# Kernel tuning notes

Hardware: AMD Instinct MI355X
Metric: run time of the kernel (lower is better)

## Reference

```python
import jax, jax.numpy as jnp
import numpy as np


def trilinear_sample(x, pts):
    """F.grid_sample 3D, mode='bilinear' (trilinear), padding_mode='border', align_corners=True.
    x: [B,C,D,H,W]; pts: [B,P,3] normalized coords in (x,y,z)=(W,H,D) order. Returns [B,C,P]."""
    B, C, D, H, W = x.shape

    def unnorm(g, size):
        # align_corners=True mapping, border padding = clamp coordinate
        return jnp.clip((g + 1.0) * 0.5 * (size - 1), 0.0, size - 1.0)

    ix = unnorm(pts[..., 0], W)
    iy = unnorm(pts[..., 1], H)
    iz = unnorm(pts[..., 2], D)
    x0 = jnp.floor(ix); y0 = jnp.floor(iy); z0 = jnp.floor(iz)
    fx = (ix - x0)[:, None, :]; fy = (iy - y0)[:, None, :]; fz = (iz - z0)[:, None, :]
    x0i = x0.astype(jnp.int32); y0i = y0.astype(jnp.int32); z0i = z0.astype(jnp.int32)
    x1i = jnp.minimum(x0i + 1, W - 1)
    y1i = jnp.minimum(y0i + 1, H - 1)
    z1i = jnp.minimum(z0i + 1, D - 1)

    xf = x.reshape(B, C, D * H * W)

    def gather(zi, yi, xi):
        idx = (zi * H + yi) * W + xi  # [B,P]
        return jnp.take_along_axis(xf, idx[:, None, :], axis=2)  # [B,C,P]

    wx0 = 1.0 - fx; wx1 = fx
    wy0 = 1.0 - fy; wy1 = fy
    wz0 = 1.0 - fz; wz1 = fz
    out = (gather(z0i, y0i, x0i) * wz0 * wy0 * wx0
           + gather(z0i, y0i, x1i) * wz0 * wy0 * wx1
           + gather(z0i, y1i, x0i) * wz0 * wy1 * wx0
           + gather(z0i, y1i, x1i) * wz0 * wy1 * wx1
           + gather(z1i, y0i, x0i) * wz1 * wy0 * wx0
           + gather(z1i, y0i, x1i) * wz1 * wy0 * wx1
           + gather(z1i, y1i, x0i) * wz1 * wy1 * wx0
           + gather(z1i, y1i, x1i) * wz1 * wy1 * wx1)
    return out


def setup_inputs() -> dict:
    key = jax.random.key(0)
    ks = jax.random.split(key, 12)
    B, C, G, N, K = 2, 64, 64, 50000, 8
    Cin = C + 3          # point_head / neighbour_head input channels
    Cd = C + 3 + 4       # delta conv input channels (features + coords + shape)
    s = 0.05
    x = jax.random.normal(ks[0], (B, C, G, G, G), jnp.float32)
    vertices = jax.random.uniform(ks[1], (B, N, 3), jnp.float32, -1.0, 1.0)
    shape_w = jax.random.normal(ks[2], (4, 4), jnp.float32) * s
    shape_b = jax.random.normal(ks[3], (4,), jnp.float32) * s
    # original init fills delta weights with 0; use small random values for a non-degenerate test
    delta_w = jax.random.normal(ks[4], (K * 3, Cd), jnp.float32) * 0.01
    delta_b = jax.random.normal(ks[5], (K * 3,), jnp.float32) * 0.01
    ph_w = jax.random.normal(ks[6], (C, Cin), jnp.float32) * s
    ph_b = jax.random.normal(ks[7], (C,), jnp.float32) * s
    nh1_w = jax.random.normal(ks[8], (C, Cin), jnp.float32) * s
    nh1_b = jax.random.normal(ks[9], (C,), jnp.float32) * s
    nh2_w = jax.random.normal(ks[10], (C, C, K + 1), jnp.float32) * s  # Conv2d kernel (1, K+1), no bias
    return {"x": x, "vertices": vertices, "shape_w": shape_w, "shape_b": shape_b,
            "delta_w": delta_w, "delta_b": delta_b, "ph_w": ph_w, "ph_b": ph_b,
            "nh1_w": nh1_w, "nh1_b": nh1_b, "nh2_w": nh2_w}


def reference(x, vertices, shape_w, shape_b, delta_w, delta_b, ph_w, ph_b, nh1_w, nh1_b, nh2_w):
    B, C, D, H, W = x.shape
    N = vertices.shape[1]
    K = delta_w.shape[0] // 3

    # sample point features
    xp = trilinear_sample(x, vertices)                                   # [B,C,N]
    cpoints = jnp.concatenate([xp, vertices.transpose(0, 2, 1)], axis=1)  # [B,C+3,N]

    # point head: 1x1 conv == per-point linear
    pfeat = jnp.einsum('oc,bcn->bno', ph_w, cpoints) + ph_b               # [B,N,C]

    # shape conditioning
    shape_vec = jnp.array([C, D, H, W], jnp.float32) @ shape_w.T + shape_b  # [4]
    sfeat = jnp.broadcast_to(shape_vec[None, :, None], (B, 4, N))
    feats = jnp.concatenate([cpoints, sfeat], axis=1)                     # [B,C+7,N]

    # learned neighbour offsets
    delta = (jnp.einsum('oc,bcn->bno', delta_w, feats) + delta_b).reshape(B, N, K, 3)
    nbrs = vertices[:, :, None, :] + delta                                # [B,N,K,3]

    # sample neighbour features
    xn = trilinear_sample(x, nbrs.reshape(B, N * K, 3)).reshape(B, C, N, K)
    cnb = jnp.concatenate([xn, nbrs.transpose(0, 3, 1, 2)], axis=1)       # [B,C+3,N,K]
    nin = jnp.concatenate([cpoints[..., None], cnb], axis=-1)             # [B,C+3,N,K+1]

    # neighbour head: 1x1 conv -> GELU -> (1,K+1) conv (reduces the K+1 axis)
    h = jax.nn.gelu(jnp.einsum('oc,bcnk->bonk', nh1_w, nin)
                    + nh1_b[None, :, None, None], approximate=False)
    nfeat = jnp.einsum('ock,bcnk->bno', nh2_w, h)                         # [B,N,C]

    return pfeat + nfeat
```

## Files before the change

### kernel.cpp

```cpp
#include <hip/hip_runtime.h>
#include <math.h>

constexpr int Bc = 2, Cc = 64, Nc = 50000, Kc = 8;
constexpr int PT = 16;
constexpr int NBLK = (Bc * Nc) / PT;

constexpr int BIAS_PH = 16;
constexpr int BIAS_N1 = 272;
constexpr int BIAS_DL = 528;
constexpr int B_PH  = 1024;
constexpr int B_N1  = 13312;
constexpr int B_DH  = 25600;
constexpr int B_DLO = 31744;
constexpr int B_N2  = 37888;
constexpr size_t XT_BYTE = 262144;
constexpr size_t XT_USHORTS = (size_t)Bc * 64 * 64 * 64 * 64;

using bf16x8 = __attribute__((ext_vector_type(8))) short;
using f32x4  = __attribute__((ext_vector_type(4))) float;

__device__ __forceinline__ float gelu_exact(float v) {
    return 0.5f * v * (1.0f + erff(v * 0.70710678118654752f));
}
__device__ __forceinline__ ushort f2bf(float f) {
    unsigned u = __float_as_uint(f);
    unsigned r = (u + 0x7FFFu + ((u >> 16) & 1u)) >> 16;
    return (ushort)r;
}
__device__ __forceinline__ float bf2f(ushort u) {
    return __uint_as_float(((unsigned)u) << 16);
}
__device__ __forceinline__ float tri8(float v000, float v001, float v010, float v011,
                                      float v100, float v101, float v110, float v111,
                                      float fx, float fy, float fz) {
    float c00 = fmaf(fx, v001 - v000, v000);
    float c01 = fmaf(fx, v011 - v010, v010);
    float c10 = fmaf(fx, v101 - v100, v100);
    float c11 = fmaf(fx, v111 - v110, v110);
    float c0  = fmaf(fy, c01 - c00, c00);
    float c1  = fmaf(fy, c11 - c10, c10);
    return fmaf(fz, c1 - c0, c0);
}

__device__ __forceinline__ void sample_pair(const unsigned* __restrict__ xtb32,
                                            ushort* __restrict__ stage,
                                            int cp, int p,
                                            float nx, float ny, float nz) {
    float ix = fminf(fmaxf((nx + 1.0f) * 31.5f, 0.0f), 63.0f);
    float iy = fminf(fmaxf((ny + 1.0f) * 31.5f, 0.0f), 63.0f);
    float iz = fminf(fmaxf((nz + 1.0f) * 31.5f, 0.0f), 63.0f);
    float fx0 = floorf(ix), fy0 = floorf(iy), fz0 = floorf(iz);
    int x0 = (int)fx0, y0 = (int)fy0, z0 = (int)fz0;
    float fx = ix - fx0, fy = iy - fy0, fz = iz - fz0;
    int dx = (x0 < 63) ? 32 : 0;
    int dy = (y0 < 63) ? 2048 : 0;
    int dz = (z0 < 63) ? 131072 : 0;
    const unsigned* r = xtb32 + ((((z0 << 12) + (y0 << 6) + x0) << 5) + cp);
    unsigned u000 = r[0],       u001 = r[dx];
    unsigned u010 = r[dy],      u011 = r[dy + dx];
    unsigned u100 = r[dz],      u101 = r[dz + dx];
    unsigned u110 = r[dz + dy], u111 = r[dz + dy + dx];
    float sa = tri8(bf2f((ushort)u000), bf2f((ushort)u001),
                    bf2f((ushort)u010), bf2f((ushort)u011),
                    bf2f((ushort)u100), bf2f((ushort)u101),
                    bf2f((ushort)u110), bf2f((ushort)u111), fx, fy, fz);
    float sb = tri8(bf2f((ushort)(u000 >> 16)), bf2f((ushort)(u001 >> 16)),
                    bf2f((ushort)(u010 >> 16)), bf2f((ushort)(u011 >> 16)),
                    bf2f((ushort)(u100 >> 16)), bf2f((ushort)(u101 >> 16)),
                    bf2f((ushort)(u110 >> 16)), bf2f((ushort)(u111 >> 16)), fx, fy, fz);
    *(unsigned*)(stage + p * 104 + 2 * cp) =
        (unsigned)f2bf(sa) | ((unsigned)f2bf(sb) << 16);
}

__device__ __forceinline__ float sample_cm(const float* __restrict__ xb,
                                           float gx, float gy, float gz) {
    float ix = fminf(fmaxf((gx + 1.0f) * 31.5f, 0.0f), 63.0f);
    float iy = fminf(fmaxf((gy + 1.0f) * 31.5f, 0.0f), 63.0f);
    float iz = fminf(fmaxf((gz + 1.0f) * 31.5f, 0.0f), 63.0f);
    float fx0 = floorf(ix), fy0 = floorf(iy), fz0 = floorf(iz);
    int x0 = (int)fx0, y0 = (int)fy0, z0 = (int)fz0;
    float fx = ix - fx0, fy = iy - fy0, fz = iz - fz0;
    int x1 = (x0 < 63) ? x0 + 1 : 63;
    int dy = (y0 < 63) ? 64 : 0;
    int dz = (z0 < 63) ? 4096 : 0;
    const float* r = xb + ((z0 << 12) + (y0 << 6));
    float v000 = r[x0],           v001 = r[x1];
    float v010 = r[x0 + dy],      v011 = r[x1 + dy];
    float v100 = r[x0 + dz],      v101 = r[x1 + dz];
    float v110 = r[x0 + dy + dz], v111 = r[x1 + dy + dz];
    return tri8(v000, v001, v010, v011, v100, v101, v110, v111, fx, fy, fz);
}

__global__ void sb_pack(const float* __restrict__ shape_w, const float* __restrict__ shape_b,
                        const float* __restrict__ delta_w, const float* __restrict__ delta_b,
                        const float* __restrict__ ph_w, const float* __restrict__ ph_b,
                        const float* __restrict__ nh1_w, const float* __restrict__ nh1_b,
                        const float* __restrict__ nh2_w, char* __restrict__ wsb) {
    int tid = blockIdx.x * blockDim.x + threadIdx.x;
    int nt  = gridDim.x * blockDim.x;
    float*  bph = (float*)(wsb + BIAS_PH);
    float*  bn1 = (float*)(wsb + BIAS_N1);
    float*  bdl = (float*)(wsb + BIAS_DL);
    ushort* wph = (ushort*)(wsb + B_PH);
    ushort* wn1 = (ushort*)(wsb + B_N1);
    ushort* wdh = (ushort*)(wsb + B_DH);
    ushort* wdl = (ushort*)(wsb + B_DLO);
    ushort* wn2 = (ushort*)(wsb + B_N2);

    for (int e = tid; e < 64; e += nt) { bph[e] = ph_b[e]; bn1[e] = nh1_b[e]; }
    for (int e = tid; e < 32; e += nt) {
        float v = 0.0f;
        if (e < 24) {
            v = delta_b[e];
#pragma unroll
            for (int i = 0; i < 4; ++i) {
                float sv = 64.0f * (shape_w[i*4] + shape_w[i*4+1] + shape_w[i*4+2] + shape_w[i*4+3])
                         + shape_b[i];
                v += sv * delta_w[e * 71 + 67 + i];
            }
        }
        bdl[e] = v;
    }
    for (int e = tid; e < 6144; e += nt) {
        int frag = e >> 9, lane = (e >> 3) & 63, j = e & 7;
        int kt = frag >> 2, n = frag & 3;
        int k = kt * 32 + ((lane >> 4) << 3) + j;
        int col = n * 16 + (lane & 15);
        wph[e] = (k < 67) ? f2bf(ph_w[col * 67 + k])  : (ushort)0;
        wn1[e] = (k < 67) ? f2bf(nh1_w[col * 67 + k]) : (ushort)0;
    }
    for (int e = tid; e < 3072; e += nt) {
        int frag = e >> 9, lane = (e >> 3) & 63, j = e & 7;
        int kt = frag >> 1, n = frag & 1;
        int k = kt * 32 + ((lane >> 4) << 3) + j;
        int col = n * 16 + (lane & 15);
        float w = (col < 24 && k < 67) ? delta_w[col * 71 + k] : 0.0f;
        ushort hi = f2bf(w);
        wdh[e] = hi;
        wdl[e] = f2bf(w - bf2f(hi));
    }
    for (int e = tid; e < 36864; e += nt) {
        int frag = e >> 9, lane = (e >> 3) & 63, j = e & 7;
        int c9 = frag >> 3, kt = (frag >> 2) & 1, n = frag & 3;
        int k = kt * 32 + ((lane >> 4) << 3) + j;
        int c = n * 16 + (lane & 15);
        wn2[e] = f2bf(nh2_w[(c * 64 + k) * 9 + c9]);
    }
}

__global__ __launch_bounds__(256) void sb_transpose(const float* __restrict__ x,
                                                    ushort* __restrict__ xt) {
    __shared__ float tile[64][65];
    int blk = blockIdx.x;
    int b = blk >> 12, zy = blk & 4095;
    const float* __restrict__ src = x + ((size_t)b << 24) + zy * 64;
    unsigned* __restrict__ dst32 = (unsigned*)(xt + ((size_t)b << 24) + (size_t)zy * 4096);
    int t = threadIdx.x;
    int xx = t & 63, c0 = t >> 6;
#pragma unroll
    for (int i = 0; i < 16; ++i) {
        int c = i * 4 + c0;
        tile[c][xx] = src[((size_t)c << 18) + xx];
    }
    __syncthreads();
    int cp = t & 31, xs0 = t >> 5;
#pragma unroll
    for (int i = 0; i < 8; ++i) {
        int xs = i * 8 + xs0;
        unsigned lo = f2bf(tile[cp * 2][xs]);
        unsigned hi = f2bf(tile[cp * 2 + 1][xs]);
        dst32[xs * 32 + cp] = lo | (hi << 16);
    }
}

__global__ __launch_bounds__(64, 6) void sb_main_mfma(
        const ushort* __restrict__ xt, const float* __restrict__ verts,
        const char* __restrict__ wsb, float* __restrict__ out) {
    __shared__ __align__(16) ushort stage[PT * 104];
    __shared__ __align__(16) ushort hst[PT * 72];
    __shared__ float pfs[PT * 64];
    __shared__ float cst[PT * 4];
    __shared__ float dls[PT * 32];

    const int lane = threadIdx.x;
    const int l15 = lane & 15, lg = lane >> 4;
    const int half8 = (lane >> 5) * 8;
    const int cp = lane & 31;
    const int g0 = blockIdx.x * PT;
    const int b  = g0 / Nc;
    const unsigned* __restrict__ xtb32 = (const unsigned*)(xt + ((size_t)b << 24));

    const float*  bph = (const float*)(wsb + BIAS_PH);
    const float*  bn1 = (const float*)(wsb + BIAS_N1);
    const float*  bdl = (const float*)(wsb + BIAS_DL);
    const ushort* Wph = (const ushort*)(wsb + B_PH);
    const ushort* Wn1 = (const ushort*)(wsb + B_N1);
    const ushort* Wdh = (const ushort*)(wsb + B_DH);
    const ushort* Wdl = (const ushort*)(wsb + B_DLO);
    const ushort* Wn2 = (const ushort*)(wsb + B_N2);

#pragma unroll
    for (int i = 0; i < (PT * 104) / 64; ++i) stage[i * 64 + lane] = 0;

    if (lane < PT) {
        const float* vp = verts + (size_t)(g0 + lane) * 3;
        float x = vp[0], y = vp[1], z = vp[2];
        cst[lane*4+0] = x; cst[lane*4+1] = y; cst[lane*4+2] = z;
        uint4 cw;
        cw.x = (unsigned)f2bf(x) | ((unsigned)f2bf(y) << 16);
        cw.y = (unsigned)f2bf(z);
        cw.z = 0u; cw.w = 0u;
        *(uint4*)(stage + lane * 104 + 64) = cw;
    }
    __syncthreads();

#pragma unroll 4
    for (int pp = 0; pp < 8; ++pp) {
        int p = half8 + pp;
        sample_pair(xtb32, stage, cp, p, cst[p*4+0], cst[p*4+1], cst[p*4+2]);
    }
    __syncthreads();

    {
        f32x4 pf[4], dd[2];
#pragma unroll
        for (int n = 0; n < 4; ++n) {
            float bp = bph[n*16 + l15];
            pf[n] = (f32x4){bp, bp, bp, bp};
        }
#pragma unroll
        for (int n = 0; n < 2; ++n) {
            float bd = bdl[n*16 + l15];
            dd[n] = (f32x4){bd, bd, bd, bd};
        }
#pragma unroll
        for (int kt = 0; kt < 3; ++kt) {
            bf16x8 a = *(const bf16x8*)(stage + l15 * 104 + kt * 32 + lg * 8);
#pragma unroll
            for (int n = 0; n < 4; ++n) {
                bf16x8 bw = *(const bf16x8*)(Wph + ((kt*4 + n) << 9) + lane * 8);
                pf[n] = __builtin_amdgcn_mfma_f32_16x16x32_bf16(a, bw, pf[n], 0, 0, 0);
            }
#pragma unroll
            for (int n = 0; n < 2; ++n) {
                bf16x8 bh = *(const bf16x8*)(Wdh + ((kt*2 + n) << 9) + lane * 8);
                dd[n] = __builtin_amdgcn_mfma_f32_16x16x32_bf16(a, bh, dd[n], 0, 0, 0);
                bf16x8 bl = *(const bf16x8*)(Wdl + ((kt*2 + n) << 9) + lane * 8);
                dd[n] = __builtin_amdgcn_mfma_f32_16x16x32_bf16(a, bl, dd[n], 0, 0, 0);
            }
        }
#pragma unroll
        for (int n = 0; n < 2; ++n)
#pragma unroll
            for (int r = 0; r < 4; ++r)
                dls[(lg*4 + r) * 32 + n*16 + l15] = dd[n][r];
#pragma unroll
        for (int n = 0; n < 4; ++n)
#pragma unroll
            for (int r = 0; r < 4; ++r)
                pfs[(lg*4 + r) * 64 + n*16 + l15] = pf[n][r];
    }

    {
        f32x4 hh[4];
#pragma unroll
        for (int n = 0; n < 4; ++n) {
            float bh = bn1[n*16 + l15];
            hh[n] = (f32x4){bh, bh, bh, bh};
        }
#pragma unroll
        for (int kt = 0; kt < 3; ++kt) {
            bf16x8 a = *(const bf16x8*)(stage + l15 * 104 + kt * 32 + lg * 8);
#pragma unroll
            for (int n = 0; n < 4; ++n) {
                bf16x8 b1 = *(const bf16x8*)(Wn1 + ((kt*4 + n) << 9) + lane * 8);
                hh[n] = __builtin_amdgcn_mfma_f32_16x16x32_bf16(a, b1, hh[n], 0, 0, 0);
            }
        }
#pragma unroll
        for (int n = 0; n < 4; ++n)
#pragma unroll
            for (int r = 0; r < 4; ++r)
                hst[(lg*4 + r) * 72 + n*16 + l15] = f2bf(gelu_exact(hh[n][r]));
    }
    __syncthreads();

    f32x4 nf[4];
#pragma unroll
    for (int n = 0; n < 4; ++n) nf[n] = (f32x4){0.f, 0.f, 0.f, 0.f};
#pragma unroll
    for (int kt = 0; kt < 2; ++kt) {
        bf16x8 a = *(const bf16x8*)(hst + l15 * 72 + kt * 32 + lg * 8);
#pragma unroll
        for (int n = 0; n < 4; ++n) {
            bf16x8 bw = *(const bf16x8*)(Wn2 + ((kt*4 + n) << 9) + lane * 8);
            nf[n] = __builtin_amdgcn_mfma_f32_16x16x32_bf16(a, bw, nf[n], 0, 0, 0);
        }
    }

    for (int k = 0; k < Kc; ++k) {
        if (lane < PT) {
            float x = cst[lane*4+0] + dls[lane*32 + 3*k + 0];
            float y = cst[lane*4+1] + dls[lane*32 + 3*k + 1];
            float z = cst[lane*4+2] + dls[lane*32 + 3*k + 2];
            uint4 cw;
            cw.x = (unsigned)f2bf(x) | ((unsigned)f2bf(y) << 16);
            cw.y = (unsigned)f2bf(z);
            cw.z = 0u; cw.w = 0u;
            *(uint4*)(stage + lane * 104 + 64) = cw;
        }
#pragma unroll 4
        for (int pp = 0; pp < 8; ++pp) {
            int p = half8 + pp;
            float nx = cst[p*4+0] + dls[p*32 + 3*k + 0];
            float ny = cst[p*4+1] + dls[p*32 + 3*k + 1];
            float nz = cst[p*4+2] + dls[p*32 + 3*k + 2];
            sample_pair(xtb32, stage, cp, p, nx, ny, nz);
        }
        __syncthreads();

        f32x4 hk[4];
#pragma unroll
        for (int n = 0; n < 4; ++n) {
            float bh = bn1[n*16 + l15];
            hk[n] = (f32x4){bh, bh, bh, bh};
        }
#pragma unroll
        for (int kt = 0; kt < 3; ++kt) {
            bf16x8 a = *(const bf16x8*)(stage + l15 * 104 + kt * 32 + lg * 8);
#pragma unroll
            for (int n = 0; n < 4; ++n) {
                bf16x8 b1 = *(const bf16x8*)(Wn1 + ((kt*4 + n) << 9) + lane * 8);
                hk[n] = __builtin_amdgcn_mfma_f32_16x16x32_bf16(a, b1, hk[n], 0, 0, 0);
            }
        }
#pragma unroll
        for (int n = 0; n < 4; ++n)
#pragma unroll
            for (int r = 0; r < 4; ++r)
                hst[(lg*4 + r) * 72 + n*16 + l15] = f2bf(gelu_exact(hk[n][r]));
        __syncthreads();

        const ushort* Wk = Wn2 + ((size_t)(k + 1) << 12);
#pragma unroll
        for (int kt = 0; kt < 2; ++kt) {
            bf16x8 a = *(const bf16x8*)(hst + l15 * 72 + kt * 32 + lg * 8);
#pragma unroll
            for (int n = 0; n < 4; ++n) {
                bf16x8 bw = *(const bf16x8*)(Wk + ((kt*4 + n) << 9) + lane * 8);
                nf[n] = __builtin_amdgcn_mfma_f32_16x16x32_bf16(a, bw, nf[n], 0, 0, 0);
            }
        }
    }

#pragma unroll
    for (int n = 0; n < 4; ++n)
#pragma unroll
        for (int r = 0; r < 4; ++r)
            out[(size_t)(g0 + lg*4 + r) * 64 + n*16 + l15] =
                pfs[(lg*4 + r) * 64 + n*16 + l15] + nf[n][r];
}

__global__ __launch_bounds__(64) void sb_fallback(
        const float* __restrict__ x, const float* __restrict__ verts,
        const float* __restrict__ shape_w, const float* __restrict__ shape_b,
        const float* __restrict__ delta_w, const float* __restrict__ delta_b,
        const float* __restrict__ ph_w, const float* __restrict__ ph_b,
        const float* __restrict__ nh1_w, const float* __restrict__ nh1_b,
        const float* __restrict__ nh2_w, float* __restrict__ out) {
    __shared__ float cp[72];
    __shared__ float hcol[64];
    __shared__ float dl[24];
    int lane = threadIdx.x;
    int g = blockIdx.x;
    int b = g / Nc;
    const float* xb = x + ((size_t)(b * 64 + lane) << 18);
    float vx = verts[g*3], vy = verts[g*3+1], vz = verts[g*3+2];
    cp[lane] = sample_cm(xb, vx, vy, vz);
    if (lane < 8) {
        float v = 0.0f;
        if      (lane == 0) v = vx;
        else if (lane == 1) v = vy;
        else if (lane == 2) v = vz;
        else if (lane < 7) {
            int i = lane - 3;
            v = 64.0f*(shape_w[i*4]+shape_w[i*4+1]+shape_w[i*4+2]+shape_w[i*4+3]) + shape_b[i];
        }
        cp[64 + lane] = v;
    }
    __syncthreads();
    float pfv = ph_b[lane];
    for (int j = 0; j < 67; ++j) pfv += ph_w[lane*67 + j] * cp[j];
    if (lane < 24) {
        float s = delta_b[lane];
        for (int j = 0; j < 71; ++j) s += delta_w[lane*71 + j] * cp[j];
        dl[lane] = s;
    }
    float h = nh1_b[lane];
    for (int j = 0; j < 67; ++j) h += nh1_w[lane*67 + j] * cp[j];
    hcol[lane] = gelu_exact(h);
    __syncthreads();
    float nfv = 0.0f;
    for (int c2 = 0; c2 < 64; ++c2) nfv += nh2_w[(lane*64 + c2)*9] * hcol[c2];
    for (int k = 0; k < 8; ++k) {
        __syncthreads();
        float nx = vx + dl[3*k], ny = vy + dl[3*k+1], nz = vz + dl[3*k+2];
        cp[lane] = sample_cm(xb, nx, ny, nz);
        if (lane < 3) cp[64 + lane] = (lane == 0) ? nx : (lane == 1) ? ny : nz;
        __syncthreads();
        float hv = nh1_b[lane];
        for (int j = 0; j < 67; ++j) hv += nh1_w[lane*67 + j] * cp[j];
        hcol[lane] = gelu_exact(hv);
        __syncthreads();
        for (int c2 = 0; c2 < 64; ++c2) nfv += nh2_w[(lane*64 + c2)*9 + k + 1] * hcol[c2];
    }
    out[(size_t)g * 64 + lane] = pfv + nfv;
}

extern "C" void kernel_launch(void* const* d_in, const int* in_sizes, int n_in,
                              void* d_out, int out_size, void* d_ws, size_t ws_size,
                              hipStream_t stream) {
    const float* x       = (const float*)d_in[0];
    const float* verts   = (const float*)d_in[1];
    const float* shape_w = (const float*)d_in[2];
    const float* shape_b = (const float*)d_in[3];
    const float* delta_w = (const float*)d_in[4];
    const float* delta_b = (const float*)d_in[5];
    const float* ph_w    = (const float*)d_in[6];
    const float* ph_b    = (const float*)d_in[7];
    const float* nh1_w   = (const float*)d_in[8];
    const float* nh1_b   = (const float*)d_in[9];
    const float* nh2_w   = (const float*)d_in[10];
    float* out = (float*)d_out;
    char*  wsb = (char*)d_ws;

    const size_t need = XT_BYTE + XT_USHORTS * 2;
    if (ws_size >= need) {
        ushort* xt = (ushort*)(wsb + XT_BYTE);
        sb_pack<<<96, 256, 0, stream>>>(shape_w, shape_b, delta_w, delta_b,
                                        ph_w, ph_b, nh1_w, nh1_b, nh2_w, wsb);
        sb_transpose<<<Bc * 4096, 256, 0, stream>>>(x, xt);
        sb_main_mfma<<<NBLK, 64, 0, stream>>>(xt, verts, wsb, out);
    } else {
        sb_fallback<<<Bc * Nc, 64, 0, stream>>>(x, verts, shape_w, shape_b, delta_w, delta_b,
                                                ph_w, ph_b, nh1_w, nh1_b, nh2_w, out);
    }
}
```

Before: 228.5 us.

## Pack two independent wave tiles per block and drop block barriers

Each 128-thread block now holds two waves. Each wave owns its own 16-point tile and its own slice of shared memory, so every __syncthreads is removed and each wave relies on in-wave ordering of its shared-memory accesses. The point-head result is no longer kept in shared memory. It is written straight to the output and read back later to add the neighbour features, which saves shared memory at the cost of an extra global read-modify-write. Occupancy hints change from 6 to 4 blocks of the larger size. Dropping the barriers risks cross-lane hazards on shared memory if the compiler reorders accesses.

```diff
diff --git a/kernel.cpp b/kernel.cpp
--- a/kernel.cpp
+++ b/kernel.cpp
@@ -3,7 +3,9 @@
 
 constexpr int Bc = 2, Cc = 64, Nc = 50000, Kc = 8;
 constexpr int PT = 16;
-constexpr int NBLK = (Bc * Nc) / PT;
+constexpr int WPB = 2;
+constexpr int NTILE = (Bc * Nc) / PT;
+constexpr int NBLK2 = NTILE / WPB;
 
 constexpr int BIAS_PH = 16;
 constexpr int BIAS_N1 = 272;
@@ -173,22 +175,28 @@
     }
 }
 
-__global__ __launch_bounds__(64, 6) void sb_main_mfma(
+__global__ __launch_bounds__(64 * WPB, 4) void sb_main_mfma(
         const ushort* __restrict__ xt, const float* __restrict__ verts,
         const char* __restrict__ wsb, float* __restrict__ out) {
-    __shared__ __align__(16) ushort stage[PT * 104];
-    __shared__ __align__(16) ushort hst[PT * 72];
-    __shared__ float pfs[PT * 64];
-    __shared__ float cst[PT * 4];
-    __shared__ float dls[PT * 32];
-
-    const int lane = threadIdx.x;
+    __shared__ __align__(16) ushort stage_s[WPB][PT * 104];
+    __shared__ __align__(16) ushort hst_s[WPB][PT * 72];
+    __shared__ float cst_s[WPB][PT * 4];
+    __shared__ float dls_s[WPB][PT * 32];
+
+    const int tid  = threadIdx.x;
+    const int wid  = tid >> 6, lane = tid & 63;
     const int l15 = lane & 15, lg = lane >> 4;
     const int half8 = (lane >> 5) * 8;
     const int cp = lane & 31;
-    const int g0 = blockIdx.x * PT;
+    const int tile = blockIdx.x * WPB + wid;
+    const int g0 = tile * PT;
     const int b  = g0 / Nc;
     const unsigned* __restrict__ xtb32 = (const unsigned*)(xt + ((size_t)b << 24));
+
+    ushort* stage = stage_s[wid];
+    ushort* hst   = hst_s[wid];
+    float*  cst   = cst_s[wid];
+    float*  dls   = dls_s[wid];
 
     const float*  bph = (const float*)(wsb + BIAS_PH);
     const float*  bn1 = (const float*)(wsb + BIAS_N1);
@@ -212,14 +220,12 @@
         cw.z = 0u; cw.w = 0u;
         *(uint4*)(stage + lane * 104 + 64) = cw;
     }
-    __syncthreads();
 
 #pragma unroll 4
     for (int pp = 0; pp < 8; ++pp) {
         int p = half8 + pp;
         sample_pair(xtb32, stage, cp, p, cst[p*4+0], cst[p*4+1], cst[p*4+2]);
     }
-    __syncthreads();
 
     {
         f32x4 pf[4], dd[2];
@@ -258,7 +264,7 @@
         for (int n = 0; n < 4; ++n)
 #pragma unroll
             for (int r = 0; r < 4; ++r)
-                pfs[(lg*4 + r) * 64 + n*16 + l15] = pf[n][r];
+                out[(size_t)(g0 + lg*4 + r) * 64 + n*16 + l15] = pf[n][r];
     }
 
     {
@@ -283,7 +289,6 @@
             for (int r = 0; r < 4; ++r)
                 hst[(lg*4 + r) * 72 + n*16 + l15] = f2bf(gelu_exact(hh[n][r]));
     }
-    __syncthreads();
 
     f32x4 nf[4];
 #pragma unroll
@@ -317,7 +322,6 @@
             float nz = cst[p*4+2] + dls[p*32 + 3*k + 2];
             sample_pair(xtb32, stage, cp, p, nx, ny, nz);
         }
-        __syncthreads();
 
         f32x4 hk[4];
 #pragma unroll
@@ -339,7 +343,6 @@
 #pragma unroll
             for (int r = 0; r < 4; ++r)
                 hst[(lg*4 + r) * 72 + n*16 + l15] = f2bf(gelu_exact(hk[n][r]));
-        __syncthreads();
 
         const ushort* Wk = Wn2 + ((size_t)(k + 1) << 12);
 #pragma unroll
@@ -356,9 +359,10 @@
 #pragma unroll
     for (int n = 0; n < 4; ++n)
 #pragma unroll
-        for (int r = 0; r < 4; ++r)
-            out[(size_t)(g0 + lg*4 + r) * 64 + n*16 + l15] =
-                pfs[(lg*4 + r) * 64 + n*16 + l15] + nf[n][r];
+        for (int r = 0; r < 4; ++r) {
+            size_t idx = (size_t)(g0 + lg*4 + r) * 64 + n*16 + l15;
+            out[idx] = out[idx] + nf[n][r];
+        }
 }
 
 __global__ __launch_bounds__(64) void sb_fallback(
@@ -440,7 +444,7 @@
         sb_pack<<<96, 256, 0, stream>>>(shape_w, shape_b, delta_w, delta_b,
                                         ph_w, ph_b, nh1_w, nh1_b, nh2_w, wsb);
         sb_transpose<<<Bc * 4096, 256, 0, stream>>>(x, xt);
-        sb_main_mfma<<<NBLK, 64, 0, stream>>>(xt, verts, wsb, out);
+        sb_main_mfma<<<NBLK2, 64 * WPB, 0, stream>>>(xt, verts, wsb, out);
     } else {
         sb_fallback<<<Bc * Nc, 64, 0, stream>>>(x, verts, shape_w, shape_b, delta_w, delta_b,
                                                 ph_w, ph_b, nh1_w, nh1_b, nh2_w, out);
```

New measurement: 294.2 us. 28.8% more time.
